# Optimization experiments

Hardware: AMD Instinct MI355X
Metric: run time of the kernel (lower is better)

Reference implementation:

```python
import jax, jax.numpy as jnp
import numpy as np

D = 64       # d_model (channel)
NHEAD = 8    # heads in nn.MultiheadAttention
PROTO = 16   # proto_size == num_queries
EPS = 1e-5


def _haar_filters():
    L = np.array([1.0, 1.0], np.float32) / np.float32(np.sqrt(2.0))
    H = np.array([-1.0, 1.0], np.float32) / np.float32(np.sqrt(2.0))
    # WavePool: LL, LH, HL, HH Haar filters (2x2, stride 2, depthwise)
    return [jnp.asarray(np.outer(a, b)) for (a, b) in ((L, L), (L, H), (H, L), (H, H))]


def _dw(x, k2d, stride):
    # depthwise conv with the SAME 2D filter per channel; x: [B,C,H,W]
    C = x.shape[1]
    k = jnp.tile(k2d[None, None], (C, 1, 1, 1)).astype(x.dtype)
    return jax.lax.conv_general_dilated(x, k, (stride, stride), 'VALID',
        dimension_numbers=('NCHW', 'OIHW', 'NCHW'), feature_group_count=C)


def _ln(x, g, b):
    m = jnp.mean(x, -1, keepdims=True)
    v = jnp.var(x, -1, keepdims=True)
    return (x - m) * jax.lax.rsqrt(v + EPS) * g + b


def _bn(x, g, b, m, v):
    # eval-mode BatchNorm2d, x: [B,C,H,W]
    sh = (1, -1, 1, 1)
    return (x - m.reshape(sh)) * jax.lax.rsqrt(v.reshape(sh) + EPS) * g.reshape(sh) + b.reshape(sh)


def _mscw(x, lw1, lb1, lw2, lb2, gw1, gb1, gw2, gb2):
    pool = jnp.mean(x, axis=1, keepdims=True)            # [B,1,C]
    loc = jax.nn.relu(x @ lw1.T + lb1) @ lw2.T + lb2
    glo = jax.nn.relu(pool @ gw1.T + gb1) @ gw2.T + gb2
    return jax.nn.sigmoid(loc + glo)


def _mha(q, k, v, w_in, b_in, w_out, b_out):
    # standard nn.MultiheadAttention (batch_first), q:[B,Nq,D], k/v:[B,Nk,D]
    B, Nq, d = q.shape
    dk = d // NHEAD
    qp = q @ w_in[:d].T + b_in[:d]
    kp = k @ w_in[d:2 * d].T + b_in[d:2 * d]
    vp = v @ w_in[2 * d:].T + b_in[2 * d:]
    split = lambda t: t.reshape(t.shape[0], t.shape[1], NHEAD, dk).transpose(0, 2, 1, 3)
    qh, kh, vh = split(qp), split(kp), split(vp)
    scores = jnp.einsum('bhqd,bhkd->bhqk', qh, kh) * (1.0 / np.sqrt(dk))
    attn = jax.nn.softmax(scores, axis=-1)
    o = jnp.einsum('bhqk,bhkd->bhqd', attn, vh).transpose(0, 2, 1, 3).reshape(B, Nq, d)
    return o @ w_out.T + b_out


def reference(tgt, memory, pos, query_pos,
              w_in, b_in, w_out, b_out,
              ln1_g, ln1_b, ln2_g, ln2_b,
              m1_lw1, m1_lb1, m1_lw2, m1_lb2, m1_gw1, m1_gb1, m1_gw2, m1_gb2,
              m2_lw1, m2_lb1, m2_lw2, m2_lb2, m2_gw1, m2_gb1, m2_gw2, m2_gb2,
              dw_w, bn1_g, bn1_b, bn1_m, bn1_v, pw_w, bn2_g, bn2_b, bn2_m, bn2_v,
              mheads_w):
    # CrossAttentionLayer.forward_post -> custom MultiheadAttention.forward
    query = (tgt + query_pos).transpose(1, 0, 2)   # [B,Nq,C]
    key = (memory + pos).transpose(1, 0, 2)        # [B,N1,C]
    value = memory.transpose(1, 0, 2)
    B, N1, C = value.shape
    hw = int(np.sqrt(N1))
    feat = key.transpose(0, 2, 1).reshape(B, C, hw, hw)
    fLL, fLH, fHL, fHH = _haar_filters()
    LL = _dw(feat, fLL, 2)
    LH = _dw(feat, fLH, 2)
    HL = _dw(feat, fHL, 2)
    HH = _dw(feat, fHH, 2)
    high = (HL + LH + HH).reshape(B, C, -1).transpose(0, 2, 1)  # [B,N1/4,C]
    low = LL.reshape(B, C, -1).transpose(0, 2, 1)
    wei = _mscw(high + low, m1_lw1, m1_lb1, m1_lw2, m1_lb2, m1_gw1, m1_gb1, m1_gw2, m1_gb2)
    fre = wei * high + low
    x1 = _mha(query, fre, fre, w_in, b_in, w_out, b_out)
    x1 = _ln(x1 + query, ln1_g, ln1_b)
    # DSConv3x3: depthwise 3x3 + BN + ReLU, then 1x1 + BN + ReLU
    y = jax.lax.conv_general_dilated(feat, dw_w, (1, 1), ((1, 1), (1, 1)),
        dimension_numbers=('NCHW', 'OIHW', 'NCHW'), feature_group_count=C)
    y = jax.nn.relu(_bn(y, bn1_g, bn1_b, bn1_m, bn1_v))
    y = jax.lax.conv_general_dilated(y, pw_w, (1, 1), 'VALID',
        dimension_numbers=('NCHW', 'OIHW', 'NCHW'))
    y = jax.nn.relu(_bn(y, bn2_g, bn2_b, bn2_m, bn2_v))
    featf = y.reshape(B, C, -1).transpose(0, 2, 1)          # [B,N1,C]
    mw = jax.nn.softmax(featf @ mheads_w.T, axis=1)          # softmax over tokens, [B,N1,P]
    protos = jnp.einsum('bnp,bnc->bpc', mw, key)             # [B,P,C]
    attn2 = _mscw(protos + query, m2_lw1, m2_lb1, m2_lw2, m2_lb2, m2_gw1, m2_gb1, m2_gw2, m2_gb2)
    x2 = _ln(query * attn2 + query, ln2_g, ln2_b)
    return (x1 + x2).transpose(1, 0, 2)                      # [Nq,B,C]


def setup_inputs() -> dict:
    key = jax.random.key(0)
    ks = iter(jax.random.split(key, 40))
    B, HW, NQ = 8, 128, PROTO
    N1 = HW * HW
    wn = lambda *s: jax.random.normal(next(ks), s, jnp.float32) * 0.05
    inp = {
        'tgt': jax.random.normal(next(ks), (NQ, B, D), jnp.float32),
        'memory': jax.random.normal(next(ks), (N1, B, D), jnp.float32),
        'pos': jax.random.normal(next(ks), (N1, B, D), jnp.float32),
        'query_pos': jax.random.normal(next(ks), (NQ, B, D), jnp.float32),
        'w_in': wn(3 * D, D), 'b_in': jnp.zeros((3 * D,), jnp.float32),
        'w_out': wn(D, D), 'b_out': jnp.zeros((D,), jnp.float32),
        'ln1_g': jnp.ones((D,), jnp.float32), 'ln1_b': jnp.zeros((D,), jnp.float32),
        'ln2_g': jnp.ones((D,), jnp.float32), 'ln2_b': jnp.zeros((D,), jnp.float32),
        'dw_w': wn(D, 1, 3, 3),
        'bn1_g': jnp.ones((D,), jnp.float32), 'bn1_b': jnp.zeros((D,), jnp.float32),
        'bn1_m': jnp.zeros((D,), jnp.float32), 'bn1_v': jnp.ones((D,), jnp.float32),
        'pw_w': wn(D, D, 1, 1),
        'bn2_g': jnp.ones((D,), jnp.float32), 'bn2_b': jnp.zeros((D,), jnp.float32),
        'bn2_m': jnp.zeros((D,), jnp.float32), 'bn2_v': jnp.ones((D,), jnp.float32),
        'mheads_w': wn(PROTO, D),
    }
    for pfx in ('m1', 'm2'):
        for br in ('l', 'g'):
            inp[f'{pfx}_{br}w1'] = wn(D, D)
            inp[f'{pfx}_{br}b1'] = jnp.zeros((D,), jnp.float32)
            inp[f'{pfx}_{br}w2'] = wn(D, D)
            inp[f'{pfx}_{br}b2'] = jnp.zeros((D,), jnp.float32)
    return inp
```

## Files before the change

### kernel.cpp

```cpp
#include <hip/hip_runtime.h>
#include <math.h>

#define N1 16384

#define OFF_KEY   0L
#define OFF_WB    4194304L
#define OFF_CST   4205056L
#define OFF_POOL  4234496L
#define OFF_PROT  4235008L
#define OFF_ZZ    4243200L
#define OFF_OSUM  4243328L
#define OFF_QP    4255616L
#define OFF_QB    4263808L

typedef __attribute__((ext_vector_type(8))) short bf16x8;
typedef __attribute__((ext_vector_type(4))) float floatx4;

#define MFMA16(a, b, c) __builtin_amdgcn_mfma_f32_16x16x32_bf16(a, b, c, 0, 0, 0)

__device__ __forceinline__ unsigned short f2bf(float f) {
    union { float f; unsigned u; } v; v.f = f;
    unsigned r = v.u + 0x7fffu + ((v.u >> 16) & 1u);
    return (unsigned short)(r >> 16);
}
__device__ __forceinline__ float bf2f(unsigned short s) {
    union { unsigned u; float f; } v; v.u = ((unsigned)s) << 16;
    return v.f;
}
__device__ __forceinline__ float sigmoidf_(float x) { return 1.f / (1.f + __expf(-x)); }
__device__ __forceinline__ bf16x8 ldg8b(const unsigned short* p) { return *(const bf16x8*)p; }
__device__ __forceinline__ void unpack8(uint4 v, float* f) {
    f[0] = bf2f((unsigned short)(v.x & 0xffff)); f[1] = bf2f((unsigned short)(v.x >> 16));
    f[2] = bf2f((unsigned short)(v.y & 0xffff)); f[3] = bf2f((unsigned short)(v.y >> 16));
    f[4] = bf2f((unsigned short)(v.z & 0xffff)); f[5] = bf2f((unsigned short)(v.z >> 16));
    f[6] = bf2f((unsigned short)(v.w & 0xffff)); f[7] = bf2f((unsigned short)(v.w >> 16));
}

__global__ __launch_bounds__(256) void k_stage1(
        const float* __restrict__ mem, const float* __restrict__ pos,
        const float* __restrict__ m1lw1, const float* __restrict__ m1lw2,
        const float* __restrict__ w_in, const float* __restrict__ pw,
        const float* __restrict__ mh, const float* __restrict__ dw_w,
        const float* __restrict__ bn1_g, const float* __restrict__ bn1_b,
        const float* __restrict__ bn1_m, const float* __restrict__ bn1_v,
        const float* __restrict__ bn2_g, const float* __restrict__ bn2_b,
        const float* __restrict__ bn2_m, const float* __restrict__ bn2_v,
        const float* __restrict__ m1gw1, const float* __restrict__ m1gw2,
        const float* __restrict__ m2gw1, const float* __restrict__ m2gw2,
        const float* __restrict__ m2lw1, const float* __restrict__ m2lw2,
        const float* __restrict__ w_out,
        const float* __restrict__ tgt, const float* __restrict__ qpos,
        const float* __restrict__ b_in,
        unsigned short* __restrict__ key, float* __restrict__ pool1raw,
        unsigned short* __restrict__ wb, float* __restrict__ cst,
        float* __restrict__ qp, float* __restrict__ queryb) {
    int tid = threadIdx.x;
    if (blockIdx.x < 4096) {
        __shared__ float sh[16][64];
        int b = blockIdx.x >> 9;
        int n_base = (blockIdx.x & 511) * 32;
        int c8 = tid & 7, local_n = tid >> 3;
        int n = n_base + local_n;
        long s4 = ((long)n * 8 + b) * 16 + c8 * 2;
        float4 m0 = ((const float4*)mem)[s4], m1 = ((const float4*)mem)[s4 + 1];
        float4 p0 = ((const float4*)pos)[s4], p1 = ((const float4*)pos)[s4 + 1];
        float f[8];
        f[0] = m0.x + p0.x; f[1] = m0.y + p0.y; f[2] = m0.z + p0.z; f[3] = m0.w + p0.w;
        f[4] = m1.x + p1.x; f[5] = m1.y + p1.y; f[6] = m1.z + p1.z; f[7] = m1.w + p1.w;
        uint4 o;
        o.x = (unsigned)f2bf(f[0]) | ((unsigned)f2bf(f[1]) << 16);
        o.y = (unsigned)f2bf(f[2]) | ((unsigned)f2bf(f[3]) << 16);
        o.z = (unsigned)f2bf(f[4]) | ((unsigned)f2bf(f[5]) << 16);
        o.w = (unsigned)f2bf(f[6]) | ((unsigned)f2bf(f[7]) << 16);
        ((uint4*)key)[(long)(b * 16384 + n) * 8 + c8] = o;
        int parity = (n_base >> 7) & 1;
        if (parity) {
            if (local_n & 1) {
                #pragma unroll
                for (int j = 0; j < 8; j++) sh[local_n >> 1][c8 * 8 + j] = f[j];
            }
            __syncthreads();
            if (tid < 64) {
                float s = 0.f;
                #pragma unroll
                for (int k = 0; k < 16; k++) s += sh[k][tid];
                atomicAdd(pool1raw + b * 64 + tid, s);
            }
        }
        return;
    }
    int blk = blockIdx.x - 4096;
    if (blk < 84) {
        int i = blk * 256 + tid;
        float v;
        if (i < 4096) v = m1lw1[i];
        else if (i < 8192) v = m1lw2[i - 4096];
        else if (i < 16384) v = w_in[4096 + (i - 8192)];
        else if (i < 20480) v = pw[i - 16384];
        else v = mh[i - 20480];
        wb[i] = f2bf(v);
    } else if (blk < 199) {
        int j = (blk - 84) * 256 + tid;
        float v;
        if (j < 576) {
            int k = j >> 6, c = j & 63;
            float s1 = bn1_g[c] * rsqrtf(bn1_v[c] + 1e-5f);
            v = dw_w[c * 9 + k] * s1;
        } else if (j < 640) {
            int c = j - 576;
            float s1 = bn1_g[c] * rsqrtf(bn1_v[c] + 1e-5f);
            v = bn1_b[c] - bn1_m[c] * s1;
        } else if (j < 704) {
            int c = j - 640;
            v = bn2_g[c] * rsqrtf(bn2_v[c] + 1e-5f);
        } else if (j < 768) {
            int c = j - 704;
            float s2 = bn2_g[c] * rsqrtf(bn2_v[c] + 1e-5f);
            v = bn2_b[c] - bn2_m[c] * s2;
        } else {
            int jj = j - 768;
            int m = jj >> 12, idx = jj & 4095;
            int sidx = (idx & 63) * 64 + (idx >> 6);
            const float* src;
            switch (m) {
                case 0: src = m1gw1; break;
                case 1: src = m1gw2; break;
                case 2: src = m2gw1; break;
                case 3: src = m2gw2; break;
                case 4: src = m2lw1; break;
                case 5: src = m2lw2; break;
                default: src = w_out; break;
            }
            v = src[sidx];
        }
        cst[j] = v;
    } else {
        __shared__ float qv[4][64];
        int g = tid >> 6, lane = tid & 63;
        int u = (blk - 199) * 4 + g;
        int b = u >> 4, q = u & 15;
        long src = ((long)q * 8 + b) * 64 + lane;
        float v = tgt[src] + qpos[src];
        qv[g][lane] = v;
        queryb[(b * 16 + q) * 64 + lane] = v;
        __syncthreads();
        float acc = b_in[lane];
        for (int cc = 0; cc < 64; cc++) acc += qv[g][cc] * w_in[lane * 64 + cc];
        qp[(b * 16 + q) * 64 + lane] = acc;
    }
}

__global__ __launch_bounds__(512) void k_stage2(
        const unsigned short* __restrict__ keyb,
        const float* __restrict__ pool1raw,
        const float* __restrict__ lb1, const float* __restrict__ lb2,
        const float* __restrict__ gb1, const float* __restrict__ gb2,
        const float* __restrict__ b_in,
        const unsigned short* __restrict__ wb,
        const float* __restrict__ cst,
        const float* __restrict__ qp,
        float* __restrict__ osum,
        float* __restrict__ protos, float* __restrict__ Z) {
    __shared__ __align__(16) char smem[63488];
    int tid = threadIdx.x;
    int w = tid >> 6, l = tid & 63;
    if (blockIdx.x < 512) {
        short* stage = (short*)smem;
        short* hbuf  = (short*)(smem + 36864);
        short* wbuf  = (short*)(smem + 46080);
        float* parr  = (float*)(smem + 55296);
        float* gtmp  = parr + 64;
        float* gbuf  = parr + 128;
        float* qs    = (float*)(smem + 56064);
        int b = blockIdx.x >> 6, tile = blockIdx.x & 63;
        int pairw = w >> 1, ch2 = w & 1;
        int m0 = pairw * 16, trow = l & 15, oct = l >> 4;
        const float* gw1T = cst + 768;
        const float* gw2T = cst + 4864;
        if (tid < 64) parr[tid] = pool1raw[b * 64 + tid] * (2.0f / 4096.0f);
        {
            int i0 = tid;
            qs[(i0 >> 6) * 68 + (i0 & 63)] = qp[(b * 16 + (i0 >> 6)) * 64 + (i0 & 63)];
            int i1 = tid + 512;
            qs[(i1 >> 6) * 68 + (i1 & 63)] = qp[(b * 16 + (i1 >> 6)) * 64 + (i1 & 63)];
        }
        const unsigned short* src = keyb + ((long)b * 16384 + tile * 256) * 64;
        #pragma unroll
        for (int k = 0; k < 4; k++) {
            int u = k * 512 + tid;
            int p = u >> 3, o = u & 7;
            uint4 v = *(const uint4*)(src + (long)u * 8);
            *(uint4*)(stage + p * 72 + o * 8) = v;
        }
        __syncthreads();
        if (tid < 64) {
            float a = gb1[tid];
            for (int cc = 0; cc < 64; cc++) a += parr[cc] * gw1T[cc * 64 + tid];
            gtmp[tid] = fmaxf(a, 0.f);
        }
        int j = m0 + trow;
        float x[16], S[16];
        bf16x8 ax[2];
        #pragma unroll
        for (int half = 0; half < 2; half++) {
            int o = oct + half * 4;
            uint4 fa4 = *(const uint4*)(stage + (2 * j) * 72 + o * 8);
            uint4 fb4 = *(const uint4*)(stage + (2 * j + 1) * 72 + o * 8);
            uint4 fc4 = *(const uint4*)(stage + (128 + 2 * j) * 72 + o * 8);
            uint4 fd4 = *(const uint4*)(stage + (129 + 2 * j) * 72 + o * 8);
            float A[8], B[8], C[8], D[8];
            unpack8(fa4, A); unpack8(fb4, B); unpack8(fc4, C); unpack8(fd4, D);
            #pragma unroll
            for (int jj = 0; jj < 8; jj++) {
                float xd = 2.f * D[jj];
                x[half * 8 + jj] = xd;
                S[half * 8 + jj] = 0.5f * (A[jj] + B[jj] + C[jj] + D[jj]);
                ax[half][jj] = (short)f2bf(xd);
            }
        }
        const unsigned short* w1b = wb;
        const unsigned short* w2b = wb + 4096;
        const unsigned short* wkb = wb + 8192;
        const unsigned short* wvb = wb + 12288;
        #pragma unroll
        for (int t4i = 0; t4i < 2; t4i++) {
            int n = (ch2 * 2 + t4i) * 16 + trow;
            float bias = lb1[n];
            floatx4 acc = {bias, bias, bias, bias};
            acc = MFMA16(ax[0], ldg8b(w1b + n * 64 + oct * 8), acc);
            acc = MFMA16(ax[1], ldg8b(w1b + n * 64 + 32 + oct * 8), acc);
            #pragma unroll
            for (int r = 0; r < 4; r++)
                hbuf[(m0 + oct * 4 + r) * 72 + n] = (short)f2bf(fmaxf(acc[r], 0.f));
        }
        __syncthreads();
        if (tid < 64) {
            float g = gb2[tid];
            for (int hh = 0; hh < 64; hh++) g += gtmp[hh] * gw2T[hh * 64 + tid];
            gbuf[tid] = g;
        }
        __syncthreads();
        {
            bf16x8 ah0 = *(const bf16x8*)(hbuf + (m0 + trow) * 72 + oct * 8);
            bf16x8 ah1 = *(const bf16x8*)(hbuf + (m0 + trow) * 72 + 32 + oct * 8);
            #pragma unroll
            for (int t4i = 0; t4i < 2; t4i++) {
                int n = (ch2 * 2 + t4i) * 16 + trow;
                float bias = lb2[n];
                floatx4 acc = {bias, bias, bias, bias};
                acc = MFMA16(ah0, ldg8b(w2b + n * 64 + oct * 8), acc);
                acc = MFMA16(ah1, ldg8b(w2b + n * 64 + 32 + oct * 8), acc);
                float g = gbuf[n];
                #pragma unroll
                for (int r = 0; r < 4; r++)
                    wbuf[(m0 + oct * 4 + r) * 72 + n] = (short)f2bf(sigmoidf_(acc[r] + g));
            }
        }
        __syncthreads();
        bf16x8 af0, af1;
        {
            bf16x8 w0 = *(const bf16x8*)(wbuf + (m0 + trow) * 72 + oct * 8);
            bf16x8 w1v = *(const bf16x8*)(wbuf + (m0 + trow) * 72 + 32 + oct * 8);
            #pragma unroll
            for (int jj = 0; jj < 8; jj++) {
                float we0 = bf2f((unsigned short)w0[jj]);
                float we1 = bf2f((unsigned short)w1v[jj]);
                af0[jj] = (short)f2bf(we0 * x[jj] + (1.f - we0) * S[jj]);
                af1[jj] = (short)f2bf(we1 * x[8 + jj] + (1.f - we1) * S[8 + jj]);
            }
        }
        __syncthreads();
        short* kbuf = hbuf; short* vbuf = wbuf;
        #pragma unroll
        for (int t4i = 0; t4i < 2; t4i++) {
            int ko = (ch2 * 2 + t4i) * 16 + trow;
            float bk = b_in[64 + ko], bv = b_in[128 + ko];
            floatx4 ak = {bk, bk, bk, bk};
            floatx4 av = {bv, bv, bv, bv};
            ak = MFMA16(af0, ldg8b(wkb + ko * 64 + oct * 8), ak);
            ak = MFMA16(af1, ldg8b(wkb + ko * 64 + 32 + oct * 8), ak);
            av = MFMA16(af0, ldg8b(wvb + ko * 64 + oct * 8), av);
            av = MFMA16(af1, ldg8b(wvb + ko * 64 + 32 + oct * 8), av);
            #pragma unroll
            for (int r = 0; r < 4; r++) {
                int row = m0 + oct * 4 + r;
                kbuf[row * 72 + ko] = (short)f2bf(ak[r]);
                vbuf[row * 72 + ko] = (short)f2bf(av[r]);
            }
        }
        __syncthreads();
        {
            int h = w;
            int q = l & 15, grp = l >> 4;
            float qf[8];
            #pragma unroll
            for (int d = 0; d < 8; d++) qf[d] = qs[q * 68 + h * 8 + d];
            const float scale = 0.35355339059327373f;
            float lsum = 0.f, acc[8];
            #pragma unroll
            for (int d = 0; d < 8; d++) acc[d] = 0.f;
            #pragma unroll
            for (int ti = 0; ti < 16; ti++) {
                int tok = grp * 16 + ti;
                uint4 k4 = *(const uint4*)(kbuf + tok * 72 + h * 8);
                uint4 v4 = *(const uint4*)(vbuf + tok * 72 + h * 8);
                float kf[8], vf[8];
                unpack8(k4, kf); unpack8(v4, vf);
                float s = qf[0] * kf[0] + qf[1] * kf[1] + qf[2] * kf[2] + qf[3] * kf[3]
                        + qf[4] * kf[4] + qf[5] * kf[5] + qf[6] * kf[6] + qf[7] * kf[7];
                float e = __expf(s * scale);
                lsum += e;
                #pragma unroll
                for (int d = 0; d < 8; d++) acc[d] += e * vf[d];
            }
            lsum += __shfl_xor(lsum, 16);
            lsum += __shfl_xor(lsum, 32);
            #pragma unroll
            for (int d = 0; d < 8; d++) {
                acc[d] += __shfl_xor(acc[d], 16);
                acc[d] += __shfl_xor(acc[d], 32);
            }
            if (grp == 0) {
                float* P = osum + ((long)((b * 8 + h) * 16 + q)) * 12;
                atomicAdd(P, lsum);
                #pragma unroll
                for (int d = 0; d < 8; d++) atomicAdd(P + 1 + d, acc[d]);
            }
        }
        return;
    }
    {
        short* stage = (short*)smem;
        short* pbuf  = (short*)(smem + 55296);
        float* cbuf  = (float*)(smem + 55296 + 4352);
        float* zred  = (float*)(smem + 55296 + 4352 + 3072);
        int blk = blockIdx.x - 512;
        int b = blk >> 7, h = blk & 127;
        int p0 = w * 16, pr = l & 15, oct = l >> 4;
        for (int k = tid; k < 768; k += 512) cbuf[k] = cst[k];
        const unsigned short* kb = keyb + (long)b * 1048576;
        #pragma unroll
        for (int r = 0; r < 3; r++) {
            int row = h - 1 + r;
            if ((unsigned)row < 128u) {
                const unsigned short* src = kb + (long)row * 8192;
                #pragma unroll
                for (int k = 0; k < 2; k++) {
                    int u = k * 512 + tid;
                    int p = u >> 3, o = u & 7;
                    uint4 v = *(const uint4*)(src + (long)u * 8);
                    *(uint4*)(stage + (r * 128 + p) * 72 + o * 8) = v;
                }
            } else {
                uint4 zz = {0u, 0u, 0u, 0u};
                #pragma unroll
                for (int k = 0; k < 2; k++) {
                    int u = k * 512 + tid;
                    int p = u >> 3, o = u & 7;
                    *(uint4*)(stage + (r * 128 + p) * 72 + o * 8) = zz;
                }
            }
        }
        __syncthreads();
        float accf[2][8];
        #pragma unroll
        for (int half = 0; half < 2; half++)
            #pragma unroll
            for (int jj = 0; jj < 8; jj++) accf[half][jj] = 0.f;
        #pragma unroll
        for (int r = 0; r < 3; r++) {
            #pragma unroll
            for (int kk = 0; kk < 3; kk++) {
                int col = p0 + pr - 1 + kk;
                if ((unsigned)col < 128u) {
                    #pragma unroll
                    for (int half = 0; half < 2; half++) {
                        int o = oct + half * 4;
                        uint4 d4 = *(const uint4*)(stage + (r * 128 + col) * 72 + o * 8);
                        float f[8]; unpack8(d4, f);
                        float4 wa = *(const float4*)(cbuf + (r * 3 + kk) * 64 + o * 8);
                        float4 wc = *(const float4*)(cbuf + (r * 3 + kk) * 64 + o * 8 + 4);
                        accf[half][0] += f[0] * wa.x; accf[half][1] += f[1] * wa.y;
                        accf[half][2] += f[2] * wa.z; accf[half][3] += f[3] * wa.w;
                        accf[half][4] += f[4] * wc.x; accf[half][5] += f[5] * wc.y;
                        accf[half][6] += f[6] * wc.z; accf[half][7] += f[7] * wc.w;
                    }
                }
            }
        }
        bf16x8 af[2];
        #pragma unroll
        for (int half = 0; half < 2; half++) {
            int o = oct + half * 4;
            float4 oa = *(const float4*)(cbuf + 576 + o * 8);
            float4 ob = *(const float4*)(cbuf + 576 + o * 8 + 4);
            af[half][0] = (short)f2bf(fmaxf(accf[half][0] + oa.x, 0.f));
            af[half][1] = (short)f2bf(fmaxf(accf[half][1] + oa.y, 0.f));
            af[half][2] = (short)f2bf(fmaxf(accf[half][2] + oa.z, 0.f));
            af[half][3] = (short)f2bf(fmaxf(accf[half][3] + oa.w, 0.f));
            af[half][4] = (short)f2bf(fmaxf(accf[half][4] + ob.x, 0.f));
            af[half][5] = (short)f2bf(fmaxf(accf[half][5] + ob.y, 0.f));
            af[half][6] = (short)f2bf(fmaxf(accf[half][6] + ob.z, 0.f));
            af[half][7] = (short)f2bf(fmaxf(accf[half][7] + ob.w, 0.f));
        }
        __syncthreads();
        short* y2buf = stage;
        short* KT = stage + 18432;
        {
            const unsigned short* pwb = wb + 16384;
            #pragma unroll
            for (int t4 = 0; t4 < 4; t4++) {
                int n = t4 * 16 + pr;
                floatx4 acc = {0.f, 0.f, 0.f, 0.f};
                acc = MFMA16(af[0], ldg8b(pwb + n * 64 + oct * 8), acc);
                acc = MFMA16(af[1], ldg8b(pwb + n * 64 + 32 + oct * 8), acc);
                float s2 = cbuf[640 + n], o2 = cbuf[704 + n];
                #pragma unroll
                for (int r = 0; r < 4; r++)
                    y2buf[(p0 + oct * 4 + r) * 72 + n] = (short)f2bf(fmaxf(acc[r] * s2 + o2, 0.f));
            }
            #pragma unroll
            for (int k2 = 0; k2 < 2; k2++) {
                int u = k2 * 512 + tid;
                int n = u >> 3, o = u & 7;
                uint4 v = *(const uint4*)(stage + (128 + n) * 72 + o * 8);
                int nx = n ^ (o << 3);
                KT[(o * 8 + 0) * 136 + nx] = (short)(v.x & 0xffff);
                KT[(o * 8 + 1) * 136 + nx] = (short)(v.x >> 16);
                KT[(o * 8 + 2) * 136 + nx] = (short)(v.y & 0xffff);
                KT[(o * 8 + 3) * 136 + nx] = (short)(v.y >> 16);
                KT[(o * 8 + 4) * 136 + nx] = (short)(v.z & 0xffff);
                KT[(o * 8 + 5) * 136 + nx] = (short)(v.z >> 16);
                KT[(o * 8 + 6) * 136 + nx] = (short)(v.w & 0xffff);
                KT[(o * 8 + 7) * 136 + nx] = (short)(v.w >> 16);
            }
        }
        __syncthreads();
        {
            const unsigned short* mhb = wb + 20480;
            bf16x8 a0 = *(const bf16x8*)(y2buf + (p0 + pr) * 72 + oct * 8);
            bf16x8 a1 = *(const bf16x8*)(y2buf + (p0 + pr) * 72 + 32 + oct * 8);
            floatx4 lg = {0.f, 0.f, 0.f, 0.f};
            lg = MFMA16(a0, ldg8b(mhb + pr * 64 + oct * 8), lg);
            lg = MFMA16(a1, ldg8b(mhb + pr * 64 + 32 + oct * 8), lg);
            float zs = 0.f;
            #pragma unroll
            for (int r = 0; r < 4; r++) {
                float e = __expf(lg[r]);
                zs += e;
                pbuf[pr * 136 + p0 + oct * 4 + r] = (short)f2bf(e);
            }
            zs += __shfl_xor(zs, 16);
            zs += __shfl_xor(zs, 32);
            if (l < 16) zred[w * 16 + l] = zs;
        }
        __syncthreads();
        if (w < 4) {
            int c = w * 16 + pr;
            int xrc = ((c >> 3) & 7) << 3;
            floatx4 acc = {0.f, 0.f, 0.f, 0.f};
            #pragma unroll
            for (int s = 0; s < 4; s++) {
                bf16x8 A = *(const bf16x8*)(pbuf + pr * 136 + s * 32 + oct * 8);
                bf16x8 B = *(const bf16x8*)(KT + c * 136 + ((s * 32 + oct * 8) ^ xrc));
                acc = MFMA16(A, B, acc);
            }
            #pragma unroll
            for (int r = 0; r < 4; r++)
                atomicAdd(protos + (b * 16 + oct * 4 + r) * 64 + c, acc[r]);
        }
        if (tid < 16) {
            float zt = 0.f;
            #pragma unroll
            for (int ww = 0; ww < 8; ww++) zt += zred[ww * 16 + tid];
            atomicAdd(Z + b * 16 + tid, zt);
        }
    }
}

__global__ __launch_bounds__(64) void k_final(
        const float* __restrict__ queryb, const float* __restrict__ protos,
        const float* __restrict__ Z, const float* __restrict__ osum,
        const float* __restrict__ cst,
        const float* __restrict__ b_out,
        const float* __restrict__ ln1_g, const float* __restrict__ ln1_b,
        const float* __restrict__ ln2_g, const float* __restrict__ ln2_b,
        const float* __restrict__ lb1, const float* __restrict__ lb2,
        const float* __restrict__ gb1, const float* __restrict__ gb2,
        float* __restrict__ out) {
    const float* gw1T = cst + 8960;
    const float* gw2T = cst + 13056;
    const float* lw1T = cst + 17152;
    const float* lw2T = cst + 21248;
    const float* woT  = cst + 25344;
    int b = blockIdx.x >> 4, t = blockIdx.x & 15;
    int c = threadIdx.x;
    __shared__ float pool[64], xsrow[64], hid[64], hidg[64], osv[64];
    float q_own = queryb[(long)(b * 16 + t) * 64 + c];
    float poolacc = 0.f, xin_own = 0.f;
    #pragma unroll
    for (int tt = 0; tt < 16; tt++) {
        float rz = 1.f / Z[b * 16 + tt];
        float xv = protos[(long)(b * 16 + tt) * 64 + c] * rz
                 + queryb[(long)(b * 16 + tt) * 64 + c];
        poolacc += xv;
        if (tt == t) xin_own = xv;
    }
    pool[c] = poolacc * (1.f / 16.f);
    xsrow[c] = xin_own;
    {
        int hh = c >> 3, d = c & 7;
        const float* P = osum + ((long)((b * 8 + hh) * 16 + t)) * 12;
        osv[c] = P[1 + d] / P[0];
    }
    __syncthreads();
    {
        float a = gb1[c], a2 = lb1[c];
        for (int cc = 0; cc < 64; cc++) {
            a  += pool[cc]  * gw1T[cc * 64 + c];
            a2 += xsrow[cc] * lw1T[cc * 64 + c];
        }
        hidg[c] = fmaxf(a, 0.f);
        hid[c]  = fmaxf(a2, 0.f);
    }
    __syncthreads();
    float glo = gb2[c], loc = lb2[c];
    for (int hh = 0; hh < 64; hh++) {
        glo += hidg[hh] * gw2T[hh * 64 + c];
        loc += hid[hh]  * lw2T[hh * 64 + c];
    }
    float attn2 = sigmoidf_(loc + glo);
    float x2p = q_own * attn2 + q_own;
    float mu = x2p;
    for (int off = 32; off; off >>= 1) mu += __shfl_down(mu, off);
    mu = __shfl(mu, 0) * (1.f / 64.f);
    float d0 = x2p - mu;
    float vv = d0 * d0;
    for (int off = 32; off; off >>= 1) vv += __shfl_down(vv, off);
    vv = __shfl(vv, 0) * (1.f / 64.f);
    float x2 = d0 * rsqrtf(vv + 1e-5f) * ln2_g[c] + ln2_b[c];
    float x1p = b_out[c];
    for (int k = 0; k < 64; k++) x1p += osv[k] * woT[k * 64 + c];
    x1p += q_own;
    float mu1 = x1p;
    for (int off = 32; off; off >>= 1) mu1 += __shfl_down(mu1, off);
    mu1 = __shfl(mu1, 0) * (1.f / 64.f);
    float d1 = x1p - mu1;
    float v1 = d1 * d1;
    for (int off = 32; off; off >>= 1) v1 += __shfl_down(v1, off);
    v1 = __shfl(v1, 0) * (1.f / 64.f);
    float x1 = d1 * rsqrtf(v1 + 1e-5f) * ln1_g[c] + ln1_b[c];
    out[((long)t * 8 + b) * 64 + c] = x1 + x2;
}

extern "C" void kernel_launch(void* const* d_in, const int* in_sizes, int n_in,
                              void* d_out, int out_size, void* d_ws, size_t ws_size,
                              hipStream_t stream) {
    const float* tgt       = (const float*)d_in[0];
    const float* memory    = (const float*)d_in[1];
    const float* pos       = (const float*)d_in[2];
    const float* query_pos = (const float*)d_in[3];
    const float* w_in      = (const float*)d_in[4];
    const float* b_in      = (const float*)d_in[5];
    const float* w_out     = (const float*)d_in[6];
    const float* b_out     = (const float*)d_in[7];
    const float* ln1_g     = (const float*)d_in[8];
    const float* ln1_b     = (const float*)d_in[9];
    const float* ln2_g     = (const float*)d_in[10];
    const float* ln2_b     = (const float*)d_in[11];
    const float* dw_w      = (const float*)d_in[12];
    const float* bn1_g     = (const float*)d_in[13];
    const float* bn1_b     = (const float*)d_in[14];
    const float* bn1_m     = (const float*)d_in[15];
    const float* bn1_v     = (const float*)d_in[16];
    const float* pw_w      = (const float*)d_in[17];
    const float* bn2_g     = (const float*)d_in[18];
    const float* bn2_b     = (const float*)d_in[19];
    const float* bn2_m     = (const float*)d_in[20];
    const float* bn2_v     = (const float*)d_in[21];
    const float* mheads    = (const float*)d_in[22];
    const float* m1_lw1 = (const float*)d_in[23];
    const float* m1_lb1 = (const float*)d_in[24];
    const float* m1_lw2 = (const float*)d_in[25];
    const float* m1_lb2 = (const float*)d_in[26];
    const float* m1_gw1 = (const float*)d_in[27];
    const float* m1_gb1 = (const float*)d_in[28];
    const float* m1_gw2 = (const float*)d_in[29];
    const float* m1_gb2 = (const float*)d_in[30];
    const float* m2_lw1 = (const float*)d_in[31];
    const float* m2_lb1 = (const float*)d_in[32];
    const float* m2_lw2 = (const float*)d_in[33];
    const float* m2_lb2 = (const float*)d_in[34];
    const float* m2_gw1 = (const float*)d_in[35];
    const float* m2_gb1 = (const float*)d_in[36];
    const float* m2_gw2 = (const float*)d_in[37];
    const float* m2_gb2 = (const float*)d_in[38];

    float* ws = (float*)d_ws;
    float* out = (float*)d_out;
    unsigned short* keyb = (unsigned short*)(ws + OFF_KEY);
    unsigned short* wb   = (unsigned short*)(ws + OFF_WB);

    hipMemsetAsync(ws + OFF_POOL, 0, 21120 * sizeof(float), stream);

    k_stage1<<<4327, 256, 0, stream>>>(memory, pos,
                                       m1_lw1, m1_lw2, w_in, pw_w, mheads, dw_w,
                                       bn1_g, bn1_b, bn1_m, bn1_v,
                                       bn2_g, bn2_b, bn2_m, bn2_v,
                                       m1_gw1, m1_gw2, m2_gw1, m2_gw2,
                                       m2_lw1, m2_lw2, w_out,
                                       tgt, query_pos, b_in,
                                       keyb, ws + OFF_POOL, wb, ws + OFF_CST,
                                       ws + OFF_QP, ws + OFF_QB);
    k_stage2<<<1536, 512, 0, stream>>>(keyb, ws + OFF_POOL,
                                       m1_lb1, m1_lb2, m1_gb1, m1_gb2, b_in,
                                       wb, ws + OFF_CST, ws + OFF_QP,
                                       ws + OFF_OSUM, ws + OFF_PROT, ws + OFF_ZZ);
    k_final<<<128, 64, 0, stream>>>(ws + OFF_QB, ws + OFF_PROT, ws + OFF_ZZ, ws + OFF_OSUM,
                                    ws + OFF_CST, b_out,
                                    ln1_g, ln1_b, ln2_g, ln2_b,
                                    m2_lb1, m2_lb2, m2_gb1, m2_gb2,
                                    out);
}
```

Measured before the change: 261.6 us.

## Split MHA attention into separate kernel with per-head K/V buffers and partial sums

Stage2 no longer computes the attention inline with atomics. It instead writes projected K and V in bf16 to head-major global buffers. A new k_mha kernel computes unnormalized softmax partials per (batch, head, segment) without atomics, and k_final reduces the 8 segment partials. This removes 9 float atomics per query per tile and the per-block q staging, at the cost of an extra kernel launch and an 8 MB K/V round trip through global memory.

Result: faster. 239.7 us (-8.4%).

```diff
diff --git a/kernel.cpp b/kernel.cpp
--- a/kernel.cpp
+++ b/kernel.cpp
@@ -4,14 +4,16 @@
 #define N1 16384
 
 #define OFF_KEY   0L
-#define OFF_WB    4194304L
-#define OFF_CST   4205056L
-#define OFF_POOL  4234496L
-#define OFF_PROT  4235008L
-#define OFF_ZZ    4243200L
-#define OFF_OSUM  4243328L
-#define OFF_QP    4255616L
-#define OFF_QB    4263808L
+#define OFF_KPH   4194304L
+#define OFF_VPH   5242880L
+#define OFF_WB    6291456L
+#define OFF_CST   6302208L
+#define OFF_POOL  6331648L
+#define OFF_PROT  6332160L
+#define OFF_ZZ    6340352L
+#define OFF_QP    6340480L
+#define OFF_QB    6348672L
+#define OFF_PART  6356864L
 
 typedef __attribute__((ext_vector_type(8))) short bf16x8;
 typedef __attribute__((ext_vector_type(4))) float floatx4;
@@ -158,8 +160,7 @@
         const float* __restrict__ b_in,
         const unsigned short* __restrict__ wb,
         const float* __restrict__ cst,
-        const float* __restrict__ qp,
-        float* __restrict__ osum,
+        unsigned short* __restrict__ kph, unsigned short* __restrict__ vph,
         float* __restrict__ protos, float* __restrict__ Z) {
     __shared__ __align__(16) char smem[63488];
     int tid = threadIdx.x;
@@ -171,19 +172,12 @@
         float* parr  = (float*)(smem + 55296);
         float* gtmp  = parr + 64;
         float* gbuf  = parr + 128;
-        float* qs    = (float*)(smem + 56064);
         int b = blockIdx.x >> 6, tile = blockIdx.x & 63;
         int pairw = w >> 1, ch2 = w & 1;
         int m0 = pairw * 16, trow = l & 15, oct = l >> 4;
         const float* gw1T = cst + 768;
         const float* gw2T = cst + 4864;
         if (tid < 64) parr[tid] = pool1raw[b * 64 + tid] * (2.0f / 4096.0f);
-        {
-            int i0 = tid;
-            qs[(i0 >> 6) * 68 + (i0 & 63)] = qp[(b * 16 + (i0 >> 6)) * 64 + (i0 & 63)];
-            int i1 = tid + 512;
-            qs[(i1 >> 6) * 68 + (i1 & 63)] = qp[(b * 16 + (i1 >> 6)) * 64 + (i1 & 63)];
-        }
         const unsigned short* src = keyb + ((long)b * 16384 + tile * 256) * 64;
         #pragma unroll
         for (int k = 0; k < 4; k++) {
@@ -290,42 +284,12 @@
         }
         __syncthreads();
         {
-            int h = w;
-            int q = l & 15, grp = l >> 4;
-            float qf[8];
-            #pragma unroll
-            for (int d = 0; d < 8; d++) qf[d] = qs[q * 68 + h * 8 + d];
-            const float scale = 0.35355339059327373f;
-            float lsum = 0.f, acc[8];
-            #pragma unroll
-            for (int d = 0; d < 8; d++) acc[d] = 0.f;
-            #pragma unroll
-            for (int ti = 0; ti < 16; ti++) {
-                int tok = grp * 16 + ti;
-                uint4 k4 = *(const uint4*)(kbuf + tok * 72 + h * 8);
-                uint4 v4 = *(const uint4*)(vbuf + tok * 72 + h * 8);
-                float kf[8], vf[8];
-                unpack8(k4, kf); unpack8(v4, vf);
-                float s = qf[0] * kf[0] + qf[1] * kf[1] + qf[2] * kf[2] + qf[3] * kf[3]
-                        + qf[4] * kf[4] + qf[5] * kf[5] + qf[6] * kf[6] + qf[7] * kf[7];
-                float e = __expf(s * scale);
-                lsum += e;
-                #pragma unroll
-                for (int d = 0; d < 8; d++) acc[d] += e * vf[d];
-            }
-            lsum += __shfl_xor(lsum, 16);
-            lsum += __shfl_xor(lsum, 32);
-            #pragma unroll
-            for (int d = 0; d < 8; d++) {
-                acc[d] += __shfl_xor(acc[d], 16);
-                acc[d] += __shfl_xor(acc[d], 32);
-            }
-            if (grp == 0) {
-                float* P = osum + ((long)((b * 8 + h) * 16 + q)) * 12;
-                atomicAdd(P, lsum);
-                #pragma unroll
-                for (int d = 0; d < 8; d++) atomicAdd(P + 1 + d, acc[d]);
-            }
+            int h = tid >> 6, tok = tid & 63;
+            uint4 kk = *(const uint4*)(kbuf + tok * 72 + h * 8);
+            uint4 vv = *(const uint4*)(vbuf + tok * 72 + h * 8);
+            long du = (long)(b * 8 + h) * 4096 + tile * 64 + tok;
+            ((uint4*)kph)[du] = kk;
+            ((uint4*)vph)[du] = vv;
         }
         return;
     }
@@ -478,9 +442,52 @@
     }
 }
 
+__global__ __launch_bounds__(256) void k_mha(const float* __restrict__ qp,
+                                             const unsigned short* __restrict__ kph,
+                                             const unsigned short* __restrict__ vph,
+                                             float* __restrict__ part) {
+    int bh = blockIdx.x >> 3, seg = blockIdx.x & 7;
+    int b = bh >> 3, hh = bh & 7;
+    int tid = threadIdx.x;
+    int q = tid >> 4, sub = tid & 15;
+    const float* qv = qp + (long)(b * 16 + q) * 64 + hh * 8;
+    float4 q0 = ((const float4*)qv)[0];
+    float4 q1 = ((const float4*)qv)[1];
+    const uint4* K4 = (const uint4*)kph + (long)bh * 4096;
+    const uint4* V4 = (const uint4*)vph + (long)bh * 4096;
+    const float scale = 0.35355339059327373f;
+    float lsum = 0.f;
+    float acc[8];
+    #pragma unroll
+    for (int d = 0; d < 8; d++) acc[d] = 0.f;
+    for (int i = 0; i < 32; i++) {
+        int n = seg * 512 + i * 16 + sub;
+        float k8[8]; unpack8(K4[n], k8);
+        float s = q0.x * k8[0] + q0.y * k8[1] + q0.z * k8[2] + q0.w * k8[3]
+                + q1.x * k8[4] + q1.y * k8[5] + q1.z * k8[6] + q1.w * k8[7];
+        float e = __expf(s * scale);
+        lsum += e;
+        float v8[8]; unpack8(V4[n], v8);
+        #pragma unroll
+        for (int d = 0; d < 8; d++) acc[d] += e * v8[d];
+    }
+    #pragma unroll
+    for (int off = 1; off < 16; off <<= 1) {
+        lsum += __shfl_xor(lsum, off);
+        #pragma unroll
+        for (int d = 0; d < 8; d++) acc[d] += __shfl_xor(acc[d], off);
+    }
+    if (sub == 0) {
+        float* P = part + ((long)(bh * 16 + q) * 8 + seg) * 12;
+        P[0] = lsum;
+        #pragma unroll
+        for (int d = 0; d < 8; d++) P[1 + d] = acc[d];
+    }
+}
+
 __global__ __launch_bounds__(64) void k_final(
         const float* __restrict__ queryb, const float* __restrict__ protos,
-        const float* __restrict__ Z, const float* __restrict__ osum,
+        const float* __restrict__ Z, const float* __restrict__ part,
         const float* __restrict__ cst,
         const float* __restrict__ b_out,
         const float* __restrict__ ln1_g, const float* __restrict__ ln1_b,
@@ -510,8 +517,14 @@
     xsrow[c] = xin_own;
     {
         int hh = c >> 3, d = c & 7;
-        const float* P = osum + ((long)((b * 8 + hh) * 16 + t)) * 12;
-        osv[c] = P[1 + d] / P[0];
+        const float* P = part + ((long)((b * 8 + hh) * 16 + t) * 8) * 12;
+        float ll = 0.f, aa = 0.f;
+        #pragma unroll
+        for (int s = 0; s < 8; s++) {
+            ll += P[s * 12];
+            aa += P[s * 12 + 1 + d];
+        }
+        osv[c] = aa / ll;
     }
     __syncthreads();
     {
@@ -599,9 +612,11 @@
     float* ws = (float*)d_ws;
     float* out = (float*)d_out;
     unsigned short* keyb = (unsigned short*)(ws + OFF_KEY);
+    unsigned short* kph  = (unsigned short*)(ws + OFF_KPH);
+    unsigned short* vph  = (unsigned short*)(ws + OFF_VPH);
     unsigned short* wb   = (unsigned short*)(ws + OFF_WB);
 
-    hipMemsetAsync(ws + OFF_POOL, 0, 21120 * sizeof(float), stream);
+    hipMemsetAsync(ws + OFF_POOL, 0, 8832 * sizeof(float), stream);
 
     k_stage1<<<4327, 256, 0, stream>>>(memory, pos,
                                        m1_lw1, m1_lw2, w_in, pw_w, mheads, dw_w,
@@ -614,9 +629,10 @@
                                        ws + OFF_QP, ws + OFF_QB);
     k_stage2<<<1536, 512, 0, stream>>>(keyb, ws + OFF_POOL,
                                        m1_lb1, m1_lb2, m1_gb1, m1_gb2, b_in,
-                                       wb, ws + OFF_CST, ws + OFF_QP,
-                                       ws + OFF_OSUM, ws + OFF_PROT, ws + OFF_ZZ);
-    k_final<<<128, 64, 0, stream>>>(ws + OFF_QB, ws + OFF_PROT, ws + OFF_ZZ, ws + OFF_OSUM,
+                                       wb, ws + OFF_CST,
+                                       kph, vph, ws + OFF_PROT, ws + OFF_ZZ);
+    k_mha<<<512, 256, 0, stream>>>(ws + OFF_QP, kph, vph, ws + OFF_PART);
+    k_final<<<128, 64, 0, stream>>>(ws + OFF_QB, ws + OFF_PROT, ws + OFF_ZZ, ws + OFF_PART,
                                     ws + OFF_CST, b_out,
                                     ln1_g, ln1_b, ln2_g, ln2_b,
                                     m2_lb1, m2_lb2, m2_gb1, m2_gb2,
```
